# Kernel optimization log

Hardware: AMD Instinct MI355X
Metric: run time of the kernel (lower is better)

Reference implementation:

```python
import jax, jax.numpy as jnp
import numpy as np

D_MODEL = 1024
D_STATE = 16
D_CONV = 4
EXPAND = 2
D_INNER = EXPAND * D_MODEL          # 2048
DT_RANK = (D_MODEL + 15) // 16      # 64 (mamba 'auto')
B, L = 2, 1024


def _mamba_params(key, scale=0.02):
    ks = jax.random.split(key, 6)
    return dict(
        inW=jax.random.normal(ks[0], (2 * D_INNER, D_MODEL), jnp.float32) * scale,
        convW=jax.random.normal(ks[1], (D_INNER, 1, D_CONV), jnp.float32) * scale,
        convb=jnp.zeros((D_INNER,), jnp.float32),
        xprojW=jax.random.normal(ks[2], (DT_RANK + 2 * D_STATE, D_INNER), jnp.float32) * scale,
        dtW=jax.random.normal(ks[3], (D_INNER, DT_RANK), jnp.float32) * scale,
        dtb=jax.random.normal(ks[4], (D_INNER,), jnp.float32) * scale,
        A_log=jnp.log(jnp.tile(jnp.arange(1, D_STATE + 1, dtype=jnp.float32), (D_INNER, 1))),
        Dskip=jnp.ones((D_INNER,), jnp.float32),
        outW=jax.random.normal(ks[5], (D_MODEL, D_INNER), jnp.float32) * scale,
    )


def setup_inputs() -> dict:
    key = jax.random.key(0)
    kx, kf, kb, kp = jax.random.split(key, 4)
    inp = {"x": jax.random.normal(kx, (B, L, D_MODEL), jnp.float32)}
    inp["ln_w"] = jnp.ones((D_MODEL,), jnp.float32)
    inp["ln_b"] = jnp.zeros((D_MODEL,), jnp.float32)
    for pref, k in (("f_", kf), ("b_", kb)):
        for name, v in _mamba_params(k).items():
            inp[pref + name] = v
    inp["proj_W"] = jax.random.normal(kp, (D_MODEL, 2 * D_MODEL), jnp.float32) * 0.02
    inp["proj_b"] = jnp.zeros((D_MODEL,), jnp.float32)
    return inp


def _layernorm(x, w, b, eps=1e-5):
    mu = jnp.mean(x, axis=-1, keepdims=True)
    var = jnp.var(x, axis=-1, keepdims=True)
    return (x - mu) * jax.lax.rsqrt(var + eps) * w + b


def _mamba(x, inW, convW, convb, xprojW, dtW, dtb, A_log, Dskip, outW):
    # x: [B, L, d_model]
    xz = jnp.einsum('bld,ed->ble', x, inW)           # [B,L,2*d_inner]
    xs, z = jnp.split(xz, 2, axis=-1)                # each [B,L,d_inner]
    # depthwise causal conv over L
    xc = jnp.transpose(xs, (0, 2, 1))                # [B,d_inner,L]
    xc = jax.lax.conv_general_dilated(
        xc, convW, window_strides=(1,), padding=[(D_CONV - 1, 0)],
        feature_group_count=D_INNER)
    xs = jax.nn.silu(jnp.transpose(xc + convb[None, :, None], (0, 2, 1)))
    # input-dependent dt, B, C
    xdb = jnp.einsum('bld,ed->ble', xs, xprojW)      # [B,L,dt_rank+2*d_state]
    dt, Bm, Cm = jnp.split(xdb, [DT_RANK, DT_RANK + D_STATE], axis=-1)
    dt = jax.nn.softplus(jnp.einsum('blr,dr->bld', dt, dtW) + dtb)  # [B,L,d_inner]
    A = -jnp.exp(A_log)                              # [d_inner,d_state], negative
    dA = jnp.exp(dt[..., None] * A)                  # [B,L,d_inner,d_state]
    dBx = dt[..., None] * Bm[:, :, None, :] * xs[..., None]

    def step(h, inputs):
        dA_t, dBx_t, C_t = inputs                    # [B,d,s],[B,d,s],[B,s]
        h = h * dA_t + dBx_t
        y = jnp.einsum('bds,bs->bd', h, C_t)
        return h, y

    h0 = jnp.zeros((x.shape[0], D_INNER, D_STATE), x.dtype)
    _, ys = jax.lax.scan(step, h0, (jnp.moveaxis(dA, 1, 0),
                                    jnp.moveaxis(dBx, 1, 0),
                                    jnp.moveaxis(Cm, 1, 0)))
    y = jnp.moveaxis(ys, 0, 1)                       # [B,L,d_inner]
    y = (y + xs * Dskip) * jax.nn.silu(z)
    return jnp.einsum('bld,ed->ble', y, outW)        # [B,L,d_model]


def reference(x, ln_w, ln_b,
              f_inW, f_convW, f_convb, f_xprojW, f_dtW, f_dtb, f_A_log, f_Dskip, f_outW,
              b_inW, b_convW, b_convb, b_xprojW, b_dtW, b_dtb, b_A_log, b_Dskip, b_outW,
              proj_W, proj_b):
    normed = _layernorm(x, ln_w, ln_b)
    fwd_out = _mamba(normed, f_inW, f_convW, f_convb, f_xprojW, f_dtW, f_dtb,
                     f_A_log, f_Dskip, f_outW)
    bwd_out = _mamba(normed[:, ::-1, :], b_inW, b_convW, b_convb, b_xprojW, b_dtW,
                     b_dtb, b_A_log, b_Dskip, b_outW)[:, ::-1, :]
    combined = jnp.concatenate([fwd_out, bwd_out], axis=-1)
    return x + jnp.einsum('blc,ec->ble', combined, proj_W) + proj_b
```

## Files before the change

kernel.cpp:

```cpp
#include <hip/hip_runtime.h>
#include <hip/hip_bf16.h>
#include <math.h>

#define DM   1024
#define DI   2048
#define DTR  64
#define DST  16
#define NB   2
#define LL   1024
#define MR   (NB*LL)
#define XLD  128
#define KS   8

typedef __bf16 bf16x8 __attribute__((ext_vector_type(8)));
typedef float  f32x4  __attribute__((ext_vector_type(4)));

__device__ __forceinline__ float siluf(float x) { return x / (1.f + __expf(-x)); }
__device__ __forceinline__ float softplusf(float x) {
    return fmaxf(x, 0.f) + log1pf(__expf(-fabsf(x)));
}
__device__ __forceinline__ unsigned short f2bf(float f) {
    __hip_bfloat16 h = __float2bfloat16(f);
    return *reinterpret_cast<unsigned short*>(&h);
}
__device__ __forceinline__ float bf2f(__hip_bfloat16 h) { return __bfloat162float(h); }

__device__ __forceinline__ void gl2lds16(const __hip_bfloat16* g, __hip_bfloat16* l)
{
    __builtin_amdgcn_global_load_lds(
        (const __attribute__((address_space(1))) unsigned int*)g,
        (__attribute__((address_space(3))) unsigned int*)l, 16, 0, 0);
}

__global__ __launch_bounds__(256) void prep_k(
    const float* __restrict__ s0, const float* __restrict__ s1,
    const float* __restrict__ s2, const float* __restrict__ s3,
    const float* __restrict__ s4, __hip_bfloat16* __restrict__ warena,
    const float* __restrict__ fx, const float* __restrict__ bx,
    __hip_bfloat16* __restrict__ wpb2,
    const float* __restrict__ fo, const float* __restrict__ bo,
    __hip_bfloat16* __restrict__ wot,
    const float* __restrict__ x, const float* __restrict__ lnw,
    const float* __restrict__ lnb, __hip_bfloat16* __restrict__ nb)
{
    __shared__ float pshm[64 * 65];
    const int b = blockIdx.x;
    const int tid = threadIdx.x;

    if (b < 10496) {
        long idx = (long)b * 1024 + tid * 4;
        const float* src; long off;
        if      (idx <  4194304L) { src = s0; off = idx; }
        else if (idx <  8388608L) { src = s1; off = idx -  4194304L; }
        else if (idx < 10485760L) { src = s2; off = idx -  8388608L; }
        else if (idx < 10616832L) { src = s3; off = idx - 10485760L; }
        else                      { src = s4; off = idx - 10616832L; }
        float4 v = *(const float4*)(src + off);
        ushort4 o;
        o.x = f2bf(v.x); o.y = f2bf(v.y); o.z = f2bf(v.z); o.w = f2bf(v.w);
        *(ushort4*)((unsigned short*)warena + idx) = o;
    } else if (b < 10624) {
        int t = b - 10496;
        int z = t >> 6;
        const float* in = z ? bx : fx;
        int idx = ((t & 63) * 256 + tid) * 4;
        int row = idx >> 11;
        ushort4 o = make_ushort4(0, 0, 0, 0);
        if (row < 96) {
            float4 v = *(const float4*)(in + idx);
            o.x = f2bf(v.x); o.y = f2bf(v.y); o.z = f2bf(v.z); o.w = f2bf(v.w);
        }
        *(ushort4*)((unsigned short*)wpb2 + (size_t)z * 128 * DI + idx) = o;
    } else if (b < 11648) {
        int t = b - 10624;
        int z = t >> 9; t &= 511;
        const float* src = z ? bo : fo;
        int c0 = (t & 31) * 64;
        int r0 = (t >> 5) * 64;
        int tc = tid & 63;
        int tr = tid >> 6;
        #pragma unroll
        for (int ii = 0; ii < 16; ++ii) {
            int rl = tr + ii * 4;
            pshm[tc * 65 + rl] = src[(size_t)(r0 + rl) * DI + c0 + tc];
        }
        __syncthreads();
        __hip_bfloat16* dst = wot + (size_t)z * DI * DM;
        #pragma unroll
        for (int ii = 0; ii < 16; ++ii) {
            int cl = tr + ii * 4;
            dst[(size_t)(c0 + cl) * DM + r0 + tc] = __float2bfloat16(pshm[cl * 65 + tc]);
        }
    } else {
        int row = b - 11648;
        const float* xr = x + (size_t)row * DM;
        float4 v = *(const float4*)(xr + tid * 4);
        float s = v.x + v.y + v.z + v.w;
        float q = v.x*v.x + v.y*v.y + v.z*v.z + v.w*v.w;
        #pragma unroll
        for (int off = 32; off > 0; off >>= 1) {
            s += __shfl_xor(s, off, 64);
            q += __shfl_xor(q, off, 64);
        }
        int wv = tid >> 6;
        if ((tid & 63) == 0) { pshm[wv] = s; pshm[8 + wv] = q; }
        __syncthreads();
        s = pshm[0] + pshm[1] + pshm[2] + pshm[3];
        q = pshm[8] + pshm[9] + pshm[10] + pshm[11];
        float mu  = s * (1.f / DM);
        float var = q * (1.f / DM) - mu * mu;
        float rstd = rsqrtf(var + 1e-5f);
        float4 wv4 = *(const float4*)(lnw + tid * 4);
        float4 bv4 = *(const float4*)(lnb + tid * 4);
        ushort4 o;
        o.x = f2bf((v.x - mu) * rstd * wv4.x + bv4.x);
        o.y = f2bf((v.y - mu) * rstd * wv4.y + bv4.y);
        o.z = f2bf((v.z - mu) * rstd * wv4.z + bv4.z);
        o.w = f2bf((v.w - mu) * rstd * wv4.w + bv4.w);
        *(ushort4*)((unsigned short*)nb + (size_t)row * DM + tid * 4) = o;
    }
}

__global__ __launch_bounds__(512) void inproj256_k(
    const __hip_bfloat16* __restrict__ A,
    const __hip_bfloat16* __restrict__ Bmat,
    __hip_bfloat16* __restrict__ C)
{
    __shared__ __hip_bfloat16 smem[65536];
    const int tid = threadIdx.x;
    int id = blockIdx.x;
    int s  = (id & 7) * 32 + (id >> 3);
    const int z  = s >> 7;
    const int r  = s & 127;
    const int bm = (r & 7) * 256;
    const int bn = (r >> 3) * 256;
    const __hip_bfloat16* Az = A;
    const __hip_bfloat16* Bz = Bmat + (size_t)z * 2 * DI * DM;
    __hip_bfloat16* Cz = C + (size_t)z * MR * 2 * DI;

    const int wv   = tid >> 6;
    const int lane = tid & 63;
    const int wm   = wv >> 2;
    const int wn   = wv & 3;
    const int fr   = lane & 15;
    const int quad = lane >> 4;

    const int r0   = tid >> 2;
    const int ksel = ((tid & 3) ^ ((r0 >> 1) & 3)) * 8;
    const int kph  = (quad ^ ((fr >> 1) & 3)) * 8;
    const int aoff = (wm * 128 + fr) * 32 + kph;
    const int boff = (wn * 64  + fr) * 32 + kph;

    __hip_bfloat16* const Asl = smem;
    __hip_bfloat16* const Bsl = smem + 32768;

    f32x4 acc[8][4] = {};

#define STG_A(T) { int q_ = (T) & 3; \
    _Pragma("unroll") for (int l = 0; l < 2; ++l) \
        gl2lds16(Az + (size_t)(bm + l * 128 + r0) * DM + (T) * 32 + ksel, \
                 Asl + q_ * 8192 + l * 4096 + wv * 512); }
#define STG_B(T) { int q_ = (T) & 3; \
    _Pragma("unroll") for (int l = 0; l < 2; ++l) \
        gl2lds16(Bz + (size_t)(bn + l * 128 + r0) * DM + (T) * 32 + ksel, \
                 Bsl + q_ * 8192 + l * 4096 + wv * 512); }

    STG_A(0); STG_B(0); STG_A(1); STG_B(1); STG_A(2); STG_B(2);

#define TILE(T, VM, DOST) { \
    asm volatile("s_barrier" ::: "memory");                \
    if (DOST) { STG_A((T) + 3); } \
    asm volatile("s_waitcnt vmcnt(" #VM ")" ::: "memory"); \
    asm volatile("s_barrier" ::: "memory");                \
    const __hip_bfloat16* At = Asl + ((T) & 3) * 8192; \
    const __hip_bfloat16* Bt = Bsl + ((T) & 3) * 8192; \
    bf16x8 bfr[4], afr[4]; \
    _Pragma("unroll") for (int j = 0; j < 4; ++j) \
        bfr[j] = *(const bf16x8*)(Bt + boff + j * 512); \
    _Pragma("unroll") for (int i = 0; i < 4; ++i) \
        afr[i] = *(const bf16x8*)(At + aoff + i * 512); \
    __builtin_amdgcn_s_setprio(1); \
    _Pragma("unroll") for (int i = 0; i < 4; ++i) \
        _Pragma("unroll") for (int j = 0; j < 4; ++j) \
            acc[i][j] = __builtin_amdgcn_mfma_f32_16x16x32_bf16( \
                afr[i], bfr[j], acc[i][j], 0, 0, 0); \
    __builtin_amdgcn_s_setprio(0); \
    if (DOST) { STG_B((T) + 3); } \
    asm volatile("s_barrier" ::: "memory");                \
    _Pragma("unroll") for (int i = 0; i < 4; ++i) \
        afr[i] = *(const bf16x8*)(At + aoff + (4 + i) * 512); \
    __builtin_amdgcn_s_setprio(1); \
    _Pragma("unroll") for (int i = 0; i < 4; ++i) \
        _Pragma("unroll") for (int j = 0; j < 4; ++j) \
            acc[4 + i][j] = __builtin_amdgcn_mfma_f32_16x16x32_bf16( \
                afr[i], bfr[j], acc[4 + i][j], 0, 0, 0); \
    __builtin_amdgcn_s_setprio(0); \
}

    for (int t = 0; t < 29; ++t) { TILE(t, 10, 1); }
    TILE(29, 8, 0);
    TILE(30, 4, 0);
    TILE(31, 0, 0);
#undef TILE
#undef STG_A
#undef STG_B

    float* eps = (float*)smem;
    const int orow = tid >> 3;
    const int ocol = (tid & 7) * 32;
    #pragma unroll
    for (int p = 0; p < 4; ++p) {
        __syncthreads();
        if (wm == (p >> 1)) {
            int ib = (p & 1) * 4;
            #pragma unroll
            for (int i2 = 0; i2 < 4; ++i2)
                #pragma unroll
                for (int j = 0; j < 4; ++j)
                    #pragma unroll
                    for (int rr = 0; rr < 4; ++rr)
                        eps[(i2 * 16 + quad * 4 + rr) * 260 + wn * 64 + j * 16 + fr]
                            = acc[ib + i2][j][rr];
        }
        __syncthreads();
        unsigned short os[32] __attribute__((aligned(16)));
        #pragma unroll
        for (int c = 0; c < 32; ++c) os[c] = f2bf(eps[orow * 260 + ocol + c]);
        unsigned short* dst = (unsigned short*)Cz +
            (size_t)(bm + p * 64 + orow) * (2 * DI) + bn + ocol;
        *(uint4*)(dst +  0) = *(const uint4*)(os +  0);
        *(uint4*)(dst +  8) = *(const uint4*)(os +  8);
        *(uint4*)(dst + 16) = *(const uint4*)(os + 16);
        *(uint4*)(dst + 24) = *(const uint4*)(os + 24);
    }
}

template<int EPI>
__global__ __launch_bounds__(256) void gemm_gl(
    const __hip_bfloat16* __restrict__ A, int lda, size_t aofs,
    const __hip_bfloat16* __restrict__ B, int ldb, size_t bofs,
    void* __restrict__ Cp, int ldc, size_t cofs, int K,
    const float* __restrict__ bias0, const float* __restrict__ bias1)
{
    __shared__ __hip_bfloat16 smem[2 * 128 * 64];
    __hip_bfloat16* As = smem;
    __hip_bfloat16* Bs = smem + 128 * 64;
    const int tid  = threadIdx.x;
    const int z    = blockIdx.z;
    const int bm   = blockIdx.y * 128;
    const int bn   = blockIdx.x * 128;
    const __hip_bfloat16* Az = A + (size_t)z * aofs;
    const __hip_bfloat16* Bz = B + (size_t)z * bofs;
    const int wv   = tid >> 6;
    const int lane = tid & 63;
    const int wr   = (wv >> 1) * 64;
    const int wc   = (wv & 1) * 64;
    const int srow = wv * 32 + (lane >> 3);
    const int cg   = ((lane & 7) ^ (lane >> 3)) * 8;
    const int fr   = lane & 15;
    const int quad = lane >> 4;
    const int pc0  = (quad ^ (fr & 7)) * 8;
    const int pc1  = ((4 + quad) ^ (fr & 7)) * 8;

    f32x4 acc[4][4] = {};

    for (int k0 = 0; k0 < K; k0 += 64) {
        __syncthreads();
        #pragma unroll
        for (int i = 0; i < 4; ++i) {
            int r = srow + i * 8;
            gl2lds16(Az + (size_t)(bm + r) * lda + k0 + cg, As + wv * 2048 + i * 512);
            gl2lds16(Bz + (size_t)(bn + r) * ldb + k0 + cg, Bs + wv * 2048 + i * 512);
        }
        __syncthreads();
        #pragma unroll
        for (int kk = 0; kk < 2; ++kk) {
            const int pc = kk ? pc1 : pc0;
            bf16x8 af[4], bf_[4];
            #pragma unroll
            for (int i = 0; i < 4; ++i) {
                af[i]  = *(const bf16x8*)(As + (wr + i * 16 + fr) * 64 + pc);
                bf_[i] = *(const bf16x8*)(Bs + (wc + i * 16 + fr) * 64 + pc);
            }
            #pragma unroll
            for (int i = 0; i < 4; ++i)
                #pragma unroll
                for (int j = 0; j < 4; ++j)
                    acc[i][j] = __builtin_amdgcn_mfma_f32_16x16x32_bf16(
                        af[i], bf_[j], acc[i][j], 0, 0, 0);
        }
    }

    const float* bias = (EPI == 3) ? (z ? bias1 : bias0) : nullptr;
    float* eps = (float*)smem;
    const int half = wv >> 1;
    const int lrow = tid >> 3;
    const int cseg = (tid & 7) * 16;
    const int gr_  = bm + (lrow >> 4) * 64 + (lrow & 15);
    #pragma unroll
    for (int i = 0; i < 4; ++i) {
        __syncthreads();
        #pragma unroll
        for (int j = 0; j < 4; ++j)
            #pragma unroll
            for (int r = 0; r < 4; ++r)
                eps[(half * 16 + quad * 4 + r) * 132 + wc + j * 16 + fr] = acc[i][j][r];
        __syncthreads();
        float vals[16];
        *(float4*)(vals +  0) = *(const float4*)(eps + lrow * 132 + cseg +  0);
        *(float4*)(vals +  4) = *(const float4*)(eps + lrow * 132 + cseg +  4);
        *(float4*)(vals +  8) = *(const float4*)(eps + lrow * 132 + cseg +  8);
        *(float4*)(vals + 12) = *(const float4*)(eps + lrow * 132 + cseg + 12);
        int gr = gr_ + i * 16;
        int gc = bn + cseg;
        if (EPI == 0) {
            float* dst = (float*)Cp + (size_t)z * cofs + (size_t)gr * ldc + gc;
            *(float4*)(dst +  0) = *(const float4*)(vals +  0);
            *(float4*)(dst +  4) = *(const float4*)(vals +  4);
            *(float4*)(dst +  8) = *(const float4*)(vals +  8);
            *(float4*)(dst + 12) = *(const float4*)(vals + 12);
        } else {
            unsigned short os[16];
            #pragma unroll
            for (int c = 0; c < 16; ++c) {
                float t = vals[c];
                if (EPI == 3) t = softplusf(t + bias[gc + c]);
                os[c] = f2bf(t);
            }
            unsigned short* dst = (unsigned short*)Cp + (size_t)z * cofs +
                                  (size_t)gr * ldc + gc;
            *(ushort4*)(dst +  0) = *(ushort4*)(os +  0);
            *(ushort4*)(dst +  4) = *(ushort4*)(os +  4);
            *(ushort4*)(dst +  8) = *(ushort4*)(os +  8);
            *(ushort4*)(dst + 12) = *(ushort4*)(os + 12);
        }
    }
}

__global__ __launch_bounds__(256) void xproj_part_k(
    const __hip_bfloat16* __restrict__ A,
    const __hip_bfloat16* __restrict__ B,
    float* __restrict__ part)
{
    __shared__ __hip_bfloat16 smem[2 * 128 * 64];
    __hip_bfloat16* As = smem;
    __hip_bfloat16* Bs = smem + 128 * 64;
    const int tid  = threadIdx.x;
    const int ks   = blockIdx.x;
    const int bm   = blockIdx.y * 128;
    const int z    = blockIdx.z;
    const __hip_bfloat16* Az = A + (size_t)z * MR * DI;
    const __hip_bfloat16* Bz = B + (size_t)z * 128 * DI;
    const int kb   = ks * (DI / KS);
    const int wv   = tid >> 6;
    const int lane = tid & 63;
    const int wr   = (wv >> 1) * 64;
    const int wc   = (wv & 1) * 64;
    const int srow = wv * 32 + (lane >> 3);
    const int cg   = ((lane & 7) ^ (lane >> 3)) * 8;
    const int fr   = lane & 15;
    const int quad = lane >> 4;
    const int pc0  = (quad ^ (fr & 7)) * 8;
    const int pc1  = ((4 + quad) ^ (fr & 7)) * 8;

    f32x4 acc[4][4] = {};

    #pragma unroll
    for (int k0 = 0; k0 < DI / KS; k0 += 64) {
        __syncthreads();
        #pragma unroll
        for (int i = 0; i < 4; ++i) {
            int r = srow + i * 8;
            gl2lds16(Az + (size_t)(bm + r) * DI + kb + k0 + cg, As + wv * 2048 + i * 512);
            gl2lds16(Bz + (size_t)r * DI + kb + k0 + cg,        Bs + wv * 2048 + i * 512);
        }
        __syncthreads();
        #pragma unroll
        for (int kk = 0; kk < 2; ++kk) {
            const int pc = kk ? pc1 : pc0;
            bf16x8 af[4], bf_[4];
            #pragma unroll
            for (int i = 0; i < 4; ++i) {
                af[i]  = *(const bf16x8*)(As + (wr + i * 16 + fr) * 64 + pc);
                bf_[i] = *(const bf16x8*)(Bs + (wc + i * 16 + fr) * 64 + pc);
            }
            #pragma unroll
            for (int i = 0; i < 4; ++i)
                #pragma unroll
                for (int j = 0; j < 4; ++j)
                    acc[i][j] = __builtin_amdgcn_mfma_f32_16x16x32_bf16(
                        af[i], bf_[j], acc[i][j], 0, 0, 0);
        }
    }

    float* dst = part + ((size_t)z * KS + ks) * MR * XLD;
    const int er = quad * 4;
    #pragma unroll
    for (int i = 0; i < 4; ++i)
        #pragma unroll
        for (int j = 0; j < 4; ++j) {
            int row = bm + wr + i * 16 + er;
            int col = wc + j * 16 + fr;
            #pragma unroll
            for (int r = 0; r < 4; ++r)
                dst[(size_t)(row + r) * XLD + col] = acc[i][j][r];
        }
}

__global__ __launch_bounds__(256) void xproj_reduce_k(
    const float* __restrict__ part, float* __restrict__ xdb,
    __hip_bfloat16* __restrict__ xdbt)
{
    int z = blockIdx.y;
    size_t idx = ((size_t)blockIdx.x * 256 + threadIdx.x) * 4;
    const float* p = part + (size_t)z * KS * MR * XLD;
    float4 s = make_float4(0.f, 0.f, 0.f, 0.f);
    #pragma unroll
    for (int ks = 0; ks < KS; ++ks) {
        float4 v = *(const float4*)(p + (size_t)ks * MR * XLD + idx);
        s.x += v.x; s.y += v.y; s.z += v.z; s.w += v.w;
    }
    *(float4*)(xdb + (size_t)z * MR * XLD + idx) = s;
    int c = (int)(idx & (XLD - 1));
    if (c < 64) {
        size_t m = idx >> 7;
        ushort4 o;
        o.x = f2bf(s.x); o.y = f2bf(s.y); o.z = f2bf(s.z); o.w = f2bf(s.w);
        *(ushort4*)((unsigned short*)xdbt + (size_t)z * MR * 64 + m * 64 + c) = o;
    }
}

__global__ __launch_bounds__(256) void conv_silu_k(
    const __hip_bfloat16* __restrict__ xz2,
    const float* __restrict__ fW, const float* __restrict__ fb,
    const float* __restrict__ bW, const float* __restrict__ bb_,
    __hip_bfloat16* __restrict__ xsb2)
{
    int dirv = blockIdx.y;
    int idx = blockIdx.x * 256 + threadIdx.x;
    int d = idx & (DI - 1);
    int m = idx >> 11;
    int t = m & (LL - 1);
    int bb = m >> 10;
    const float* w  = (dirv ? bW : fW) + d * 4;
    const __hip_bfloat16* xz = xz2 + (size_t)dirv * MR * 2 * DI;
    float acc = (dirv ? bb_ : fb)[d];
    if (dirv == 0) {
        #pragma unroll
        for (int k = 0; k < 4; ++k) {
            int tt = t - 3 + k;
            if (tt >= 0)
                acc = fmaf(w[k], bf2f(xz[(size_t)(bb * LL + tt) * (2 * DI) + d]), acc);
        }
    } else {
        #pragma unroll
        for (int k = 0; k < 4; ++k) {
            int tt = t + 3 - k;
            if (tt < LL)
                acc = fmaf(w[k], bf2f(xz[(size_t)(bb * LL + tt) * (2 * DI) + d]), acc);
        }
    }
    xsb2[(size_t)dirv * MR * DI + (size_t)m * DI + d] = __float2bfloat16(siluf(acc));
}

__global__ __launch_bounds__(256) void scan1_k(
    const __hip_bfloat16* __restrict__ dtf2, const __hip_bfloat16* __restrict__ xsb2,
    const float* __restrict__ xdb2,
    const float* __restrict__ fA, const float* __restrict__ bA,
    float* __restrict__ hend, float* __restrict__ aprod, int G, int Cn)
{
    int d  = blockIdx.x * 256 + threadIdx.x;
    int bb = blockIdx.y;
    int zz = blockIdx.z;
    int dirv = (zz >= G) ? 1 : 0;
    int g = zz - (dirv ? G : 0);
    const float* A_log = dirv ? bA : fA;
    const __hip_bfloat16* dtf = dtf2 + (size_t)dirv * MR * DI;
    const __hip_bfloat16* xs = xsb2 + (size_t)dirv * MR * DI;
    const float* xdb = xdb2 + (size_t)dirv * MR * XLD;
    size_t hoff = (size_t)dirv * G * (NB * DI * DST);

    float Ad[DST], h[DST], ap[DST];
    bool pw = true;
    #pragma unroll
    for (int s = 0; s < DST; ++s) {
        Ad[s] = -__expf(A_log[d * DST + s]);
        pw = pw && (fabsf(Ad[s] + (float)(s + 1)) < 1e-3f * (s + 1));
        h[s] = 0.f; ap[s] = 1.f;
    }
    int i0 = g * Cn;
    for (int i = 0; i < Cn; ++i) {
        int ii = i0 + i;
        int t = dirv ? (LL - 1 - ii) : ii;
        size_t m = (size_t)bb * LL + t;
        float dtv = bf2f(dtf[m * DI + d]);
        float xv  = bf2f(xs[m * DI + d]);
        const float* bc = xdb + m * XLD;
        float dtx = dtv * xv;
        float dAv[DST];
        if (pw) {
            float r = __expf(-dtv);
            float a = r;
            #pragma unroll
            for (int s = 0; s < DST; ++s) { dAv[s] = a; a *= r; }
        } else {
            #pragma unroll
            for (int s = 0; s < DST; ++s) dAv[s] = __expf(dtv * Ad[s]);
        }
        #pragma unroll
        for (int s = 0; s < DST; ++s) {
            h[s] = fmaf(h[s], dAv[s], dtx * bc[64 + s]);
            ap[s] *= dAv[s];
        }
    }
    size_t base = hoff + ((size_t)(g * NB + bb) * DI + d) * DST;
    #pragma unroll
    for (int s = 0; s < DST; s += 4) {
        *(float4*)(hend  + base + s) = make_float4(h[s], h[s+1], h[s+2], h[s+3]);
        *(float4*)(aprod + base + s) = make_float4(ap[s], ap[s+1], ap[s+2], ap[s+3]);
    }
}

__global__ __launch_bounds__(256) void scan2_k(
    float* __restrict__ hend, const float* __restrict__ aprod, int G)
{
    int dirv = blockIdx.y;
    int idx = blockIdx.x * 256 + threadIdx.x;
    const int slab = NB * DI * DST;
    size_t hoff = (size_t)dirv * G * slab;
    float carry = 0.f;
    for (int g = 0; g < G; ++g) {
        size_t off = hoff + (size_t)g * slab + idx;
        float a = aprod[off];
        float e = hend[off];
        hend[off] = carry;
        carry = fmaf(a, carry, e);
    }
}

__global__ __launch_bounds__(256) void scan3_k(
    const __hip_bfloat16* __restrict__ dtf2, const __hip_bfloat16* __restrict__ xsb2,
    const float* __restrict__ xdb2, const __hip_bfloat16* __restrict__ xz2,
    const float* __restrict__ fA, const float* __restrict__ bA,
    const float* __restrict__ fD, const float* __restrict__ bD,
    const float* __restrict__ hin, __hip_bfloat16* __restrict__ ycat, int G, int Cn)
{
    int d  = blockIdx.x * 256 + threadIdx.x;
    int bb = blockIdx.y;
    int zz = blockIdx.z;
    int dirv = (zz >= G) ? 1 : 0;
    int g = zz - (dirv ? G : 0);
    const float* A_log = dirv ? bA : fA;
    const float* Dskip = dirv ? bD : fD;
    const __hip_bfloat16* dtf = dtf2 + (size_t)dirv * MR * DI;
    const __hip_bfloat16* xs = xsb2 + (size_t)dirv * MR * DI;
    const float* xdb = xdb2 + (size_t)dirv * MR * XLD;
    const __hip_bfloat16* xz = xz2 + (size_t)dirv * MR * 2 * DI;
    size_t hoff = (size_t)dirv * G * (NB * DI * DST);

    float Ad[DST], h[DST];
    bool pw = true;
    size_t base = hoff + ((size_t)(g * NB + bb) * DI + d) * DST;
    #pragma unroll
    for (int s = 0; s < DST; ++s) {
        Ad[s] = -__expf(A_log[d * DST + s]);
        pw = pw && (fabsf(Ad[s] + (float)(s + 1)) < 1e-3f * (s + 1));
        h[s] = hin[base + s];
    }
    float Dsk = Dskip[d];
    int i0 = g * Cn;
    for (int i = 0; i < Cn; ++i) {
        int ii = i0 + i;
        int t = dirv ? (LL - 1 - ii) : ii;
        size_t m = (size_t)bb * LL + t;
        float dtv = bf2f(dtf[m * DI + d]);
        float xv  = bf2f(xs[m * DI + d]);
        const float* bc = xdb + m * XLD;
        float dtx = dtv * xv;
        float dAv[DST];
        if (pw) {
            float r = __expf(-dtv);
            float a = r;
            #pragma unroll
            for (int s = 0; s < DST; ++s) { dAv[s] = a; a *= r; }
        } else {
            #pragma unroll
            for (int s = 0; s < DST; ++s) dAv[s] = __expf(dtv * Ad[s]);
        }
        float yv = 0.f;
        #pragma unroll
        for (int s = 0; s < DST; ++s) {
            h[s] = fmaf(h[s], dAv[s], dtx * bc[64 + s]);
            yv = fmaf(h[s], bc[80 + s], yv);
        }
        float zv = bf2f(xz[m * (2 * DI) + DI + d]);
        ycat[m * (2 * DI) + (size_t)dirv * DI + d] =
            __float2bfloat16((yv + xv * Dsk) * siluf(zv));
    }
}

__global__ __launch_bounds__(256) void scan_mono_k(
    const __hip_bfloat16* __restrict__ dtf2, const __hip_bfloat16* __restrict__ xsb2,
    const float* __restrict__ xdb2, const __hip_bfloat16* __restrict__ xz2,
    const float* __restrict__ fA, const float* __restrict__ bA,
    const float* __restrict__ fD, const float* __restrict__ bD,
    __hip_bfloat16* __restrict__ ycat)
{
    int d  = blockIdx.x * 256 + threadIdx.x;
    int bb = blockIdx.y;
    int dirv = blockIdx.z;
    const float* A_log = dirv ? bA : fA;
    const float* Dskip = dirv ? bD : fD;
    const __hip_bfloat16* dtf = dtf2 + (size_t)dirv * MR * DI;
    const __hip_bfloat16* xs = xsb2 + (size_t)dirv * MR * DI;
    const float* xdb = xdb2 + (size_t)dirv * MR * XLD;
    const __hip_bfloat16* xz = xz2 + (size_t)dirv * MR * 2 * DI;
    float Ad[DST], h[DST];
    #pragma unroll
    for (int s = 0; s < DST; ++s) { Ad[s] = -__expf(A_log[d * DST + s]); h[s] = 0.f; }
    float Dsk = Dskip[d];
    for (int i = 0; i < LL; ++i) {
        int t = dirv ? (LL - 1 - i) : i;
        size_t m = (size_t)bb * LL + t;
        float dtv = bf2f(dtf[m * DI + d]);
        float xv  = bf2f(xs[m * DI + d]);
        const float* bc = xdb + m * XLD;
        float dtx = dtv * xv;
        float yv = 0.f;
        #pragma unroll
        for (int s = 0; s < DST; ++s) {
            float dA = __expf(dtv * Ad[s]);
            h[s] = fmaf(h[s], dA, dtx * bc[64 + s]);
            yv = fmaf(h[s], bc[80 + s], yv);
        }
        float zv = bf2f(xz[m * (2 * DI) + DI + d]);
        ycat[m * (2 * DI) + (size_t)dirv * DI + d] =
            __float2bfloat16((yv + xv * Dsk) * siluf(zv));
    }
}

__global__ __launch_bounds__(256) void final_reduce_k(
    const float* __restrict__ part, const float* __restrict__ x,
    const float* __restrict__ proj_b, float* __restrict__ out)
{
    size_t idx = ((size_t)blockIdx.x * 256 + threadIdx.x) * 4;
    float4 s = make_float4(0.f, 0.f, 0.f, 0.f);
    #pragma unroll
    for (int z = 0; z < 4; ++z) {
        float4 v = *(const float4*)(part + (size_t)z * MR * DM + idx);
        s.x += v.x; s.y += v.y; s.z += v.z; s.w += v.w;
    }
    float4 xv = *(const float4*)(x + idx);
    float4 pb = *(const float4*)(proj_b + (idx & (DM - 1)));
    float4 o;
    o.x = xv.x + pb.x + s.x;
    o.y = xv.y + pb.y + s.y;
    o.z = xv.z + pb.z + s.z;
    o.w = xv.w + pb.w + s.w;
    *(float4*)(out + idx) = o;
}

extern "C" void kernel_launch(void* const* d_in, const int* in_sizes, int n_in,
                              void* d_out, int out_size, void* d_ws, size_t ws_size,
                              hipStream_t stream)
{
    const float* x      = (const float*)d_in[0];
    const float* ln_w   = (const float*)d_in[1];
    const float* ln_b   = (const float*)d_in[2];
    const float* f_inW    = (const float*)d_in[3];
    const float* f_convW  = (const float*)d_in[4];
    const float* f_convb  = (const float*)d_in[5];
    const float* f_xprojW = (const float*)d_in[6];
    const float* f_dtW    = (const float*)d_in[7];
    const float* f_dtb    = (const float*)d_in[8];
    const float* f_A_log  = (const float*)d_in[9];
    const float* f_Dskip  = (const float*)d_in[10];
    const float* f_outW   = (const float*)d_in[11];
    const float* b_inW    = (const float*)d_in[12];
    const float* b_convW  = (const float*)d_in[13];
    const float* b_convb  = (const float*)d_in[14];
    const float* b_xprojW = (const float*)d_in[15];
    const float* b_dtW    = (const float*)d_in[16];
    const float* b_dtb    = (const float*)d_in[17];
    const float* b_A_log  = (const float*)d_in[18];
    const float* b_Dskip  = (const float*)d_in[19];
    const float* b_outW   = (const float*)d_in[20];
    const float* proj_W = (const float*)d_in[21];
    const float* proj_b = (const float*)d_in[22];

    float* ws = (float*)d_ws;
    size_t o = 0;
    __hip_bfloat16* xz2  = (__hip_bfloat16*)(ws + o);
    float* fpart = ws + o;
    o += (size_t)2 * MR * 2 * DI / 2;
    __hip_bfloat16* xsb2 = (__hip_bfloat16*)(ws + o); o += (size_t)2 * MR * DI / 2;
    __hip_bfloat16* ycat = (__hip_bfloat16*)(ws + o);
    float* xpart = ws + o;
    o += (size_t)MR * 2 * DI / 2;
    float* xdb2 = ws + o; o += (size_t)2 * MR * XLD;
    __hip_bfloat16* xdbt = (__hip_bfloat16*)(ws + o); o += (size_t)2 * MR * 64 / 2;
    __hip_bfloat16* dtfb = (__hip_bfloat16*)(ws + o); o += (size_t)2 * MR * DI / 2;
    __hip_bfloat16* nb = (__hip_bfloat16*)(ws + o); o += (size_t)MR * DM / 2;
    __hip_bfloat16* warena = (__hip_bfloat16*)(ws + o); o += 15466496 / 2;
    float* hbuf = ws + o;
    size_t base_floats = o;

    __hip_bfloat16* wbi  = warena;
    __hip_bfloat16* pwb  = warena +  8388608;
    __hip_bfloat16* wdt  = warena + 10485760;
    __hip_bfloat16* wpb2 = warena + 10747904;
    __hip_bfloat16* wcat = warena + 11272192;

    const size_t slab = (size_t)NB * DI * DST;
    int G = 32;
    while (G > 4 && (base_floats + 4ull * G * slab) * 4 > ws_size) G >>= 1;
    int useChunks = ((base_floats + 4ull * G * slab) * 4 <= ws_size);
    float* hend  = hbuf;
    float* aprod = hbuf + 2ull * G * slab;
    int Cn = useChunks ? LL / G : LL;

    int wotInHbuf = useChunks && (4ull * G * slab >= 2097152ull);
    __hip_bfloat16* wot = wotInHbuf ? (__hip_bfloat16*)hbuf : xz2;

    prep_k<<<13696, 256, 0, stream>>>(
        f_inW, b_inW, proj_W, f_dtW, b_dtW, warena,
        f_xprojW, b_xprojW, wpb2,
        f_outW, b_outW, wot,
        x, ln_w, ln_b, nb);

    if (wotInHbuf) {
        inproj256_k<<<256, 512, 0, stream>>>(nb, wbi, xz2);
        gemm_gl<1><<<dim3(DI / 128, DM / 128, 2), 256, 0, stream>>>(
            pwb, 2 * DM, (size_t)DM, wot, DM, (size_t)DI * DM,
            wcat, 2 * DI, (size_t)DI, DM, nullptr, nullptr);
    } else {
        gemm_gl<1><<<dim3(DI / 128, DM / 128, 2), 256, 0, stream>>>(
            pwb, 2 * DM, (size_t)DM, wot, DM, (size_t)DI * DM,
            wcat, 2 * DI, (size_t)DI, DM, nullptr, nullptr);
        inproj256_k<<<256, 512, 0, stream>>>(nb, wbi, xz2);
    }

    conv_silu_k<<<dim3((MR * DI) / 256, 2), 256, 0, stream>>>(
        xz2, f_convW, f_convb, b_convW, b_convb, xsb2);

    xproj_part_k<<<dim3(KS, MR / 128, 2), 256, 0, stream>>>(xsb2, wpb2, xpart);
    xproj_reduce_k<<<dim3((MR * XLD) / 1024, 2), 256, 0, stream>>>(xpart, xdb2, xdbt);

    gemm_gl<3><<<dim3(DI / 128, MR / 128, 2), 256, 0, stream>>>(
        xdbt, 64, (size_t)MR * 64, wdt, 64, (size_t)DI * 64,
        dtfb, DI, (size_t)MR * DI, 64, f_dtb, b_dtb);

    if (useChunks) {
        scan1_k<<<dim3(DI / 256, NB, 2 * G), 256, 0, stream>>>(
            dtfb, xsb2, xdb2, f_A_log, b_A_log, hend, aprod, G, Cn);
        scan2_k<<<dim3((NB * DI * DST) / 256, 2), 256, 0, stream>>>(hend, aprod, G);
        scan3_k<<<dim3(DI / 256, NB, 2 * G), 256, 0, stream>>>(
            dtfb, xsb2, xdb2, xz2, f_A_log, b_A_log, f_Dskip, b_Dskip,
            hend, ycat, G, Cn);
    } else {
        scan_mono_k<<<dim3(DI / 256, NB, 2), 256, 0, stream>>>(
            dtfb, xsb2, xdb2, xz2, f_A_log, b_A_log, f_Dskip, b_Dskip, ycat);
    }

    gemm_gl<0><<<dim3(DM / 128, MR / 128, 4), 256, 0, stream>>>(
        ycat, 2 * DI, 1024, wcat, 2 * DI, 1024,
        fpart, DM, (size_t)MR * DM, 1024, nullptr, nullptr);

    final_reduce_k<<<(MR * DM) / 1024, 256, 0, stream>>>(
        fpart, x, proj_b, (float*)d_out);
}
```

Before: 422.3 us.

## Software-pipeline LDS fragment reads across k-tiles in in_proj GEMM

Restructures the GEMM main loop so the next tile's B and low-half A fragments are read from LDS while the current tile's high-half MFMAs run, using double-buffered B register sets. Global-to-LDS staging is rescheduled to interleave with the MFMA phases, with adjusted waitcnt/barrier placement. The aim is to hide LDS read latency behind matrix ops, at the cost of more live registers, which could reduce occupancy or cause spills.

```diff
diff --git a/kernel.cpp b/kernel.cpp
--- a/kernel.cpp
+++ b/kernel.cpp
@@ -155,6 +155,7 @@
     __hip_bfloat16* const Bsl = smem + 32768;
 
     f32x4 acc[8][4] = {};
+    bf16x8 aL[4], aH[4], b0[4], b1[4];
 
 #define STG_A(T) { int q_ = (T) & 3; \
     _Pragma("unroll") for (int l = 0; l < 2; ++l) \
@@ -165,43 +166,70 @@
         gl2lds16(Bz + (size_t)(bn + l * 128 + r0) * DM + (T) * 32 + ksel, \
                  Bsl + q_ * 8192 + l * 4096 + wv * 512); }
 
-    STG_A(0); STG_B(0); STG_A(1); STG_B(1); STG_A(2); STG_B(2);
-
-#define TILE(T, VM, DOST) { \
-    asm volatile("s_barrier" ::: "memory");                \
-    if (DOST) { STG_A((T) + 3); } \
-    asm volatile("s_waitcnt vmcnt(" #VM ")" ::: "memory"); \
-    asm volatile("s_barrier" ::: "memory");                \
-    const __hip_bfloat16* At = Asl + ((T) & 3) * 8192; \
-    const __hip_bfloat16* Bt = Bsl + ((T) & 3) * 8192; \
-    bf16x8 bfr[4], afr[4]; \
+#define RD_AL(T) { const __hip_bfloat16* p_ = Asl + ((T) & 3) * 8192; \
+    _Pragma("unroll") for (int i = 0; i < 4; ++i) \
+        aL[i] = *(const bf16x8*)(p_ + aoff + i * 512); }
+#define RD_AH(T) { const __hip_bfloat16* p_ = Asl + ((T) & 3) * 8192; \
+    _Pragma("unroll") for (int i = 0; i < 4; ++i) \
+        aH[i] = *(const bf16x8*)(p_ + aoff + (4 + i) * 512); }
+#define RD_B(T, BV) { const __hip_bfloat16* p_ = Bsl + ((T) & 3) * 8192; \
     _Pragma("unroll") for (int j = 0; j < 4; ++j) \
-        bfr[j] = *(const bf16x8*)(Bt + boff + j * 512); \
-    _Pragma("unroll") for (int i = 0; i < 4; ++i) \
-        afr[i] = *(const bf16x8*)(At + aoff + i * 512); \
+        BV[j] = *(const bf16x8*)(p_ + boff + j * 512); }
+
+#define MFMA_LO(BV) \
     __builtin_amdgcn_s_setprio(1); \
     _Pragma("unroll") for (int i = 0; i < 4; ++i) \
         _Pragma("unroll") for (int j = 0; j < 4; ++j) \
             acc[i][j] = __builtin_amdgcn_mfma_f32_16x16x32_bf16( \
-                afr[i], bfr[j], acc[i][j], 0, 0, 0); \
-    __builtin_amdgcn_s_setprio(0); \
-    if (DOST) { STG_B((T) + 3); } \
-    asm volatile("s_barrier" ::: "memory");                \
-    _Pragma("unroll") for (int i = 0; i < 4; ++i) \
-        afr[i] = *(const bf16x8*)(At + aoff + (4 + i) * 512); \
+                aL[i], BV[j], acc[i][j], 0, 0, 0); \
+    __builtin_amdgcn_s_setprio(0);
+#define MFMA_HI(BV) \
     __builtin_amdgcn_s_setprio(1); \
     _Pragma("unroll") for (int i = 0; i < 4; ++i) \
         _Pragma("unroll") for (int j = 0; j < 4; ++j) \
             acc[4 + i][j] = __builtin_amdgcn_mfma_f32_16x16x32_bf16( \
-                afr[i], bfr[j], acc[4 + i][j], 0, 0, 0); \
-    __builtin_amdgcn_s_setprio(0); \
-}
-
-    for (int t = 0; t < 29; ++t) { TILE(t, 10, 1); }
-    TILE(29, 8, 0);
-    TILE(30, 4, 0);
-    TILE(31, 0, 0);
-#undef TILE
+                aH[i], BV[j], acc[4 + i][j], 0, 0, 0); \
+    __builtin_amdgcn_s_setprio(0);
+
+#define PH0(T, BCUR, SB) { \
+    asm volatile("s_barrier" ::: "memory"); \
+    RD_AH(T); \
+    MFMA_LO(BCUR); \
+    if (SB) { STG_B((T) + 3); } }
+
+#define PH1(T, BCUR, BNXT, VMS, SA, R3) { \
+    asm volatile("s_waitcnt " VMS ::: "memory"); \
+    asm volatile("s_barrier" ::: "memory"); \
+    if (R3) { RD_B((T) + 1, BNXT); RD_AL((T) + 1); } \
+    MFMA_HI(BCUR); \
+    if (SA) { STG_A((T) + 4); } }
+
+    STG_A(0); STG_B(0); STG_A(1); STG_B(1); STG_A(2); STG_B(2);
+    asm volatile("s_waitcnt vmcnt(8)" ::: "memory");
+    asm volatile("s_barrier" ::: "memory");
+    RD_B(0, b0); RD_AL(0);
+    STG_A(3);
+
+    #pragma unroll 1
+    for (int u = 0; u < 13; ++u) {
+        const int t0 = 2 * u;
+        PH0(t0, b0, 1);     PH1(t0, b0, b1, "vmcnt(8)", 1, 1);
+        PH0(t0 + 1, b1, 1); PH1(t0 + 1, b1, b0, "vmcnt(8)", 1, 1);
+    }
+    PH0(26, b0, 1); PH1(26, b0, b1, "vmcnt(8)", 1, 1);
+    PH0(27, b1, 1); PH1(27, b1, b0, "vmcnt(8)", 1, 1);
+    PH0(28, b0, 1); PH1(28, b0, b1, "vmcnt(8)", 0, 1);
+    PH0(29, b1, 0); PH1(29, b1, b0, "vmcnt(4)", 0, 1);
+    PH0(30, b0, 0); PH1(30, b0, b1, "vmcnt(0)", 0, 1);
+    PH0(31, b1, 0); PH1(31, b1, b0, "vmcnt(0)", 0, 0);
+
+#undef PH0
+#undef PH1
+#undef MFMA_LO
+#undef MFMA_HI
+#undef RD_AL
+#undef RD_AH
+#undef RD_B
 #undef STG_A
 #undef STG_B
 
```

Measured after the change: 419.0 us. Within noise of the previous version (-0.8%).

## Repipeline in-projection GEMM with half-K phases and vectorize conv-SiLU kernel

Applied to the files above, without the earlier changes.

The 256x256 in-projection GEMM main loop is restructured from a 4-deep ring of 32-wide K tiles into a double-buffered 64-wide step split into four phases. Each phase interleaves one LDS fragment read, one global-to-LDS stage and 16 MFMAs, with explicit lgkmcnt/vmcnt waits and sched barriers, aiming to hide load latency better and cut barrier overhead. Separately, the depthwise conv+SiLU kernel now makes each thread handle 8 channels, using vector loads and one 16-byte store, with an 8x smaller grid. The new pipeline has tighter wait-count bookkeeping, which risks races if the counts are off.

```diff
diff --git a/kernel.cpp b/kernel.cpp
--- a/kernel.cpp
+++ b/kernel.cpp
@@ -24,6 +24,10 @@
     return *reinterpret_cast<unsigned short*>(&h);
 }
 __device__ __forceinline__ float bf2f(__hip_bfloat16 h) { return __bfloat162float(h); }
+__device__ __forceinline__ float bfu2f(unsigned short u) {
+    __hip_bfloat16 h = *reinterpret_cast<__hip_bfloat16*>(&u);
+    return __bfloat162float(h);
+}
 
 __device__ __forceinline__ void gl2lds16(const __hip_bfloat16* g, __hip_bfloat16* l)
 {
@@ -145,63 +149,82 @@
     const int fr   = lane & 15;
     const int quad = lane >> 4;
 
-    const int r0   = tid >> 2;
-    const int ksel = ((tid & 3) ^ ((r0 >> 1) & 3)) * 8;
+    const int srow = tid >> 2;
+    const int scol = 8 * ((tid & 3) ^ ((tid >> 3) & 3));
     const int kph  = (quad ^ ((fr >> 1) & 3)) * 8;
-    const int aoff = (wm * 128 + fr) * 32 + kph;
-    const int boff = (wn * 64  + fr) * 32 + kph;
 
     __hip_bfloat16* const Asl = smem;
     __hip_bfloat16* const Bsl = smem + 32768;
 
     f32x4 acc[8][4] = {};
-
-#define STG_A(T) { int q_ = (T) & 3; \
-    _Pragma("unroll") for (int l = 0; l < 2; ++l) \
-        gl2lds16(Az + (size_t)(bm + l * 128 + r0) * DM + (T) * 32 + ksel, \
-                 Asl + q_ * 8192 + l * 4096 + wv * 512); }
-#define STG_B(T) { int q_ = (T) & 3; \
-    _Pragma("unroll") for (int l = 0; l < 2; ++l) \
-        gl2lds16(Bz + (size_t)(bn + l * 128 + r0) * DM + (T) * 32 + ksel, \
-                 Bsl + q_ * 8192 + l * 4096 + wv * 512); }
-
-    STG_A(0); STG_B(0); STG_A(1); STG_B(1); STG_A(2); STG_B(2);
-
-#define TILE(T, VM, DOST) { \
-    asm volatile("s_barrier" ::: "memory");                \
-    if (DOST) { STG_A((T) + 3); } \
-    asm volatile("s_waitcnt vmcnt(" #VM ")" ::: "memory"); \
-    asm volatile("s_barrier" ::: "memory");                \
-    const __hip_bfloat16* At = Asl + ((T) & 3) * 8192; \
-    const __hip_bfloat16* Bt = Bsl + ((T) & 3) * 8192; \
-    bf16x8 bfr[4], afr[4]; \
+    bf16x8 aF[4], bB[4];
+
+#define STG_A(TAU, KK) { \
+    const int ub_ = (((TAU) & 1) * 2 + (KK)) * 8192; \
+    const int gc_ = (TAU) * 64 + (KK) * 32 + scol; \
+    gl2lds16(Az + (size_t)(bm + srow) * DM + gc_,       Asl + ub_ + tid * 8); \
+    gl2lds16(Az + (size_t)(bm + 128 + srow) * DM + gc_, Asl + ub_ + 4096 + tid * 8); }
+#define STG_B(TAU, KK) { \
+    const int ub_ = (((TAU) & 1) * 2 + (KK)) * 8192; \
+    const int gc_ = (TAU) * 64 + (KK) * 32 + scol; \
+    gl2lds16(Bz + (size_t)(bn + srow) * DM + gc_,       Bsl + ub_ + tid * 8); \
+    gl2lds16(Bz + (size_t)(bn + 128 + srow) * DM + gc_, Bsl + ub_ + 4096 + tid * 8); }
+
+#define RD_A(BUF, KK, MH) { \
+    const __hip_bfloat16* p_ = Asl + ((BUF) * 2 + (KK)) * 8192 + kph; \
+    _Pragma("unroll") for (int i = 0; i < 4; ++i) \
+        aF[i] = *(const bf16x8*)(p_ + (wm * 128 + (MH) * 64 + i * 16 + fr) * 32); }
+#define RD_B(BUF, KK) { \
+    const __hip_bfloat16* p_ = Bsl + ((BUF) * 2 + (KK)) * 8192 + kph; \
     _Pragma("unroll") for (int j = 0; j < 4; ++j) \
-        bfr[j] = *(const bf16x8*)(Bt + boff + j * 512); \
-    _Pragma("unroll") for (int i = 0; i < 4; ++i) \
-        afr[i] = *(const bf16x8*)(At + aoff + i * 512); \
+        bB[j] = *(const bf16x8*)(p_ + (wn * 64 + j * 16 + fr) * 32); }
+
+#define PHASE(BUF, KK, MH, STGC, T1, T2, VMC) { \
+    if ((MH) == 0) { RD_B(BUF, KK); } \
+    RD_A(BUF, KK, MH); \
+    if ((STGC) == 1) { STG_A((T1), 1); } \
+    if ((STGC) == 2) { STG_B((T1), 1); } \
+    if ((STGC) == 3) { STG_A((T2), 0); } \
+    if ((STGC) == 4) { STG_B((T2), 0); } \
+    asm volatile("s_barrier" ::: "memory"); \
+    asm volatile("s_waitcnt lgkmcnt(0)" ::: "memory"); \
+    __builtin_amdgcn_sched_barrier(0); \
     __builtin_amdgcn_s_setprio(1); \
     _Pragma("unroll") for (int i = 0; i < 4; ++i) \
         _Pragma("unroll") for (int j = 0; j < 4; ++j) \
-            acc[i][j] = __builtin_amdgcn_mfma_f32_16x16x32_bf16( \
-                afr[i], bfr[j], acc[i][j], 0, 0, 0); \
+            acc[(MH) * 4 + i][j] = __builtin_amdgcn_mfma_f32_16x16x32_bf16( \
+                aF[i], bB[j], acc[(MH) * 4 + i][j], 0, 0, 0); \
     __builtin_amdgcn_s_setprio(0); \
-    if (DOST) { STG_B((T) + 3); } \
-    asm volatile("s_barrier" ::: "memory");                \
-    _Pragma("unroll") for (int i = 0; i < 4; ++i) \
-        afr[i] = *(const bf16x8*)(At + aoff + (4 + i) * 512); \
-    __builtin_amdgcn_s_setprio(1); \
-    _Pragma("unroll") for (int i = 0; i < 4; ++i) \
-        _Pragma("unroll") for (int j = 0; j < 4; ++j) \
-            acc[4 + i][j] = __builtin_amdgcn_mfma_f32_16x16x32_bf16( \
-                afr[i], bfr[j], acc[4 + i][j], 0, 0, 0); \
-    __builtin_amdgcn_s_setprio(0); \
-}
-
-    for (int t = 0; t < 29; ++t) { TILE(t, 10, 1); }
-    TILE(29, 8, 0);
-    TILE(30, 4, 0);
-    TILE(31, 0, 0);
-#undef TILE
+    if ((VMC) == 8) { asm volatile("s_waitcnt vmcnt(8)" ::: "memory"); } \
+    if ((VMC) == 4) { asm volatile("s_waitcnt vmcnt(4)" ::: "memory"); } \
+    if ((VMC) == 1) { asm volatile("s_waitcnt vmcnt(0)" ::: "memory"); } \
+    asm volatile("s_barrier" ::: "memory"); }
+
+    STG_A(0, 0); STG_B(0, 0); STG_A(0, 1); STG_B(0, 1); STG_A(1, 0); STG_B(1, 0);
+    asm volatile("s_waitcnt vmcnt(8)" ::: "memory");
+    asm volatile("s_barrier" ::: "memory");
+
+    #pragma unroll 1
+    for (int t = 0; t < 14; ++t) {
+        const int buf = t & 1;
+        const int t1 = t + 1, t2 = t + 2;
+        PHASE(buf, 0, 0, 1, t1, t2, 0);
+        PHASE(buf, 0, 1, 2, t1, t2, 8);
+        PHASE(buf, 1, 0, 3, t1, t2, 0);
+        PHASE(buf, 1, 1, 4, t1, t2, 8);
+    }
+    PHASE(0, 0, 0, 1, 15, 0, 0);
+    PHASE(0, 0, 1, 2, 15, 0, 8);
+    PHASE(0, 1, 0, 0, 0, 0, 0);
+    PHASE(0, 1, 1, 0, 0, 0, 4);
+    PHASE(1, 0, 0, 0, 0, 0, 0);
+    PHASE(1, 0, 1, 0, 0, 0, 1);
+    PHASE(1, 1, 0, 0, 0, 0, 0);
+    PHASE(1, 1, 1, 0, 0, 0, 0);
+
+#undef PHASE
+#undef RD_A
+#undef RD_B
 #undef STG_A
 #undef STG_B
 
@@ -437,30 +460,40 @@
     __hip_bfloat16* __restrict__ xsb2)
 {
     int dirv = blockIdx.y;
-    int idx = blockIdx.x * 256 + threadIdx.x;
+    int idx = (blockIdx.x * 256 + threadIdx.x) * 8;
     int d = idx & (DI - 1);
     int m = idx >> 11;
     int t = m & (LL - 1);
     int bb = m >> 10;
-    const float* w  = (dirv ? bW : fW) + d * 4;
-    const __hip_bfloat16* xz = xz2 + (size_t)dirv * MR * 2 * DI;
-    float acc = (dirv ? bb_ : fb)[d];
-    if (dirv == 0) {
-        #pragma unroll
-        for (int k = 0; k < 4; ++k) {
-            int tt = t - 3 + k;
-            if (tt >= 0)
-                acc = fmaf(w[k], bf2f(xz[(size_t)(bb * LL + tt) * (2 * DI) + d]), acc);
-        }
-    } else {
-        #pragma unroll
-        for (int k = 0; k < 4; ++k) {
-            int tt = t + 3 - k;
-            if (tt < LL)
-                acc = fmaf(w[k], bf2f(xz[(size_t)(bb * LL + tt) * (2 * DI) + d]), acc);
-        }
-    }
-    xsb2[(size_t)dirv * MR * DI + (size_t)m * DI + d] = __float2bfloat16(siluf(acc));
+    const float* w    = (dirv ? bW : fW) + d * 4;
+    const float* bias = (dirv ? bb_ : fb) + d;
+    const __hip_bfloat16* xz = xz2 + (size_t)dirv * MR * 2 * DI + d;
+    float acc[8];
+    #pragma unroll
+    for (int c = 0; c < 8; ++c) acc[c] = bias[c];
+    #pragma unroll
+    for (int k = 0; k < 4; ++k) {
+        int tt = dirv ? (t + 3 - k) : (t - 3 + k);
+        bool ok = dirv ? (tt < LL) : (tt >= 0);
+        if (ok) {
+            const unsigned short* row =
+                (const unsigned short*)(xz + (size_t)(bb * LL + tt) * (2 * DI));
+            ushort4 v0 = *(const ushort4*)(row + 0);
+            ushort4 v1 = *(const ushort4*)(row + 4);
+            acc[0] = fmaf(w[0 * 4 + k], bfu2f(v0.x), acc[0]);
+            acc[1] = fmaf(w[1 * 4 + k], bfu2f(v0.y), acc[1]);
+            acc[2] = fmaf(w[2 * 4 + k], bfu2f(v0.z), acc[2]);
+            acc[3] = fmaf(w[3 * 4 + k], bfu2f(v0.w), acc[3]);
+            acc[4] = fmaf(w[4 * 4 + k], bfu2f(v1.x), acc[4]);
+            acc[5] = fmaf(w[5 * 4 + k], bfu2f(v1.y), acc[5]);
+            acc[6] = fmaf(w[6 * 4 + k], bfu2f(v1.z), acc[6]);
+            acc[7] = fmaf(w[7 * 4 + k], bfu2f(v1.w), acc[7]);
+        }
+    }
+    unsigned short o[8] __attribute__((aligned(16)));
+    #pragma unroll
+    for (int c = 0; c < 8; ++c) o[c] = f2bf(siluf(acc[c]));
+    *(uint4*)((unsigned short*)xsb2 + (size_t)dirv * MR * DI + idx) = *(const uint4*)o;
 }
 
 __global__ __launch_bounds__(256) void scan1_k(
@@ -740,7 +773,7 @@
         inproj256_k<<<256, 512, 0, stream>>>(nb, wbi, xz2);
     }
 
-    conv_silu_k<<<dim3((MR * DI) / 256, 2), 256, 0, stream>>>(
+    conv_silu_k<<<dim3((MR * DI) / 2048, 2), 256, 0, stream>>>(
         xz2, f_convW, f_convb, b_convW, b_convb, xsb2);
 
     xproj_part_k<<<dim3(KS, MR / 128, 2), 256, 0, stream>>>(xsb2, wpb2, xpart);
```

New measurement: 446.3 us. 1.06x slower.
